# Kernel optimization log

Hardware: AMD Instinct MI355X
Metric: run time of the kernel (lower is better)

Reference implementation:

```python
import jax, jax.numpy as jnp
import numpy as np

N = 8192
NUM_CLASSES = 5
DIM = 3
EPS = 15.0
MIN_POINTS = 5
N_BATCH = 2


def setup_inputs() -> dict:
    key = jax.random.key(0)
    k1, k2, k3, k4 = jax.random.split(key, 4)
    # coords in a 96^3 box so eps=15 neighborhoods contain > minPoints same-group points
    coords = jax.random.uniform(k1, (N, DIM)) * 96.0
    batch = jax.random.randint(k2, (N, 1), 0, N_BATCH).astype(jnp.float32)
    feat = jax.random.normal(k3, (N, 1))
    seg = jax.random.normal(k4, (N, NUM_CLASSES))
    x = jnp.concatenate([coords, batch, feat, seg], axis=1).astype(jnp.float32)
    return {"x": x}


def _dbscan_labels(x):
    """Per-point DBSCAN cluster labels, run independently per (batch, class) group.
    noise = -1; cluster ids start at 0 within each group, ordered by the smallest
    point index of each cluster's core component (matches the serial scan order
    of the original implementation). Border points get the smallest adjacent
    cluster id (= first cluster to reach them in the serial algorithm)."""
    data = x[:, :-NUM_CLASSES]                 # (N, dim+2)
    seg = x[:, -NUM_CLASSES:]                  # (N, C)
    cls = jnp.argmax(seg, axis=1).astype(jnp.int32)
    b = data[:, DIM].astype(jnp.int32)
    pts = data[:, :DIM]                        # (N, 3)
    group = b * NUM_CLASSES + cls              # (N,) group id per point

    # pairwise squared distances via gram trick; d < eps  <=>  d2 < eps^2
    p2 = jnp.sum(pts * pts, axis=1)
    d2 = p2[:, None] + p2[None, :] - 2.0 * (pts @ pts.T)
    same = group[:, None] == group[None, :]
    adj = same & (d2 < EPS * EPS)              # includes self (d2 ~ 0)
    core = jnp.sum(adj, axis=1) >= MIN_POINTS  # region_query counts self too
    adjcc = adj & core[:, None] & core[None, :]

    idx = jnp.arange(N, dtype=jnp.int32)
    SENT = jnp.int32(N)
    lab0 = jnp.where(core, idx, SENT)

    # connected components of core-core graph via min-label propagation + pointer jumping
    def cond(st):
        return st[1]

    def body(st):
        lab, _ = st
        m = jnp.min(jnp.where(adjcc, lab[None, :], SENT), axis=1)
        nl = jnp.minimum(lab, m)
        safe = jnp.where(core, nl, 0)          # nl < N for core points
        nl2 = jnp.where(core, jnp.minimum(nl, nl[safe]), SENT)
        return (nl2, jnp.any(nl2 != lab))

    rep, _ = jax.lax.while_loop(cond, body, (lab0, jnp.array(True)))

    # per-group sequential cluster ids, ordered by component representative index
    is_rep = core & (rep == idx)
    cid_of_rep = jnp.zeros((N,), jnp.int32)
    for g in range(N_BATCH * NUM_CLASSES):     # fixed small count of groups
        mg = is_rep & (group == g)
        cum = jnp.cumsum(mg.astype(jnp.int32))
        cid_of_rep = jnp.where(mg, cum - 1, cid_of_rep)
    core_cid = cid_of_rep[jnp.where(core, rep, 0)]

    # border points: min cluster id among adjacent core points (same group via adj)
    nb_core = adj & core[None, :]
    BIG = jnp.int32(2 ** 30)
    bcid = jnp.min(jnp.where(nb_core, core_cid[None, :], BIG), axis=1)
    has_core_nb = jnp.any(nb_core, axis=1)
    labels = jnp.where(core, core_cid, jnp.where(has_core_nb, bcid, -1))
    return labels


def reference(x):
    labels = _dbscan_labels(x)
    data = x[:, :-NUM_CLASSES]
    # fixed-shape equivalent of the cluster gather: clustered points keep their
    # data columns (the differentiable part of the original output), noise zeroed
    clustered = jnp.where(labels[:, None] >= 0, data, 0.0)
    return labels, clustered
```

## Files before the change

### kernel.cpp

```cpp
#include <hip/hip_runtime.h>
#include <cstdint>
#include <cstddef>

#define NPTS 8192
#define NWORDS 128
#define NUM_CLASSES 5
#define XCOLS 10
#define MIN_PTS 5
#define NGROUPS 10
#define BIGC 0x3fffffff

#define NLCAP 1536
#define EACAP 8192
#define ELCAP 8192
#define EBCAP 2048
#define CPAD 64
#define NSLICE 24
#define PTHREADS 512
#define PWAVES 8
#define GTHREADS 1024
#define ROUNDS 16

__global__ void k_init(const float* __restrict__ x, int* __restrict__ grp,
                       unsigned int* __restrict__ gcnt) {
    int i = blockIdx.x * blockDim.x + threadIdx.x;
    if (i < NGROUPS * CPAD) gcnt[i] = 0u;
    if (i >= NPTS) return;
    const float2* r2 = (const float2*)(x + (size_t)i * XCOLS);
    float2 c23 = r2[1];
    float2 c45 = r2[2];
    float2 c67 = r2[3];
    float2 c89 = r2[4];
    float best = c45.y; int bc = 0;
    if (c67.x > best) { best = c67.x; bc = 1; }
    if (c67.y > best) { best = c67.y; bc = 2; }
    if (c89.x > best) { best = c89.x; bc = 3; }
    if (c89.y > best) { best = c89.y; bc = 4; }
    grp[i] = (int)c23.y * NUM_CLASSES + bc;
}

__global__ void __launch_bounds__(PTHREADS) k_pairs(
        const float* __restrict__ x, const int* __restrict__ grp,
        unsigned int* __restrict__ eAll_g, unsigned int* __restrict__ gcnt,
        int* __restrict__ deg_g, int* __restrict__ nlist_g, int* __restrict__ nn_g) {
    __shared__ float4 pts[NLCAP];
    __shared__ unsigned long long masks[NWORDS];
    __shared__ int pref[NWORDS];
    __shared__ int srowdeg[64];
    __shared__ int nnS;

    const int g = blockIdx.x / NSLICE;
    const int s = blockIdx.x % NSLICE;
    const int tid = threadIdx.x, lane = tid & 63, wv = tid >> 6;

    for (int k = tid; k < NLCAP; k += PTHREADS)
        pts[k] = make_float4(0.f, 0.f, 0.f, 1.0e38f);
    if (tid < 64) srowdeg[tid] = 0;
    for (int w = wv; w < NWORDS; w += PWAVES) {
        unsigned long long bm = __ballot(grp[w * 64 + lane] == g);
        if (lane == 0) masks[w] = bm;
    }
    __syncthreads();
    if (wv == 0) {
        int v0 = __popcll(masks[lane]);
        int incl = v0;
        #pragma unroll
        for (int st = 1; st < 64; st <<= 1) {
            int o = __shfl_up(incl, st);
            if (lane >= st) incl += o;
        }
        pref[lane] = incl - v0;
        int tot0 = __shfl(incl, 63);
        int v1 = __popcll(masks[64 + lane]);
        int incl1 = v1;
        #pragma unroll
        for (int st = 1; st < 64; st <<= 1) {
            int o = __shfl_up(incl1, st);
            if (lane >= st) incl1 += o;
        }
        pref[64 + lane] = tot0 + incl1 - v1;
        if (lane == 63) nnS = tot0 + incl1;
    }
    __syncthreads();
    for (int w = wv; w < NWORDS; w += PWAVES) {
        unsigned long long bm = masks[w];
        if ((bm >> lane) & 1ull) {
            int p = pref[w] + __popcll(bm & ((1ull << lane) - 1ull));
            if (p < NLCAP) {
                int i = w * 64 + lane;
                const float2* r2 = (const float2*)(x + (size_t)i * XCOLS);
                float2 c01 = r2[0]; float2 c23 = r2[1];
                float px = c01.x, py = c01.y, pz = c23.x;
                pts[p] = make_float4(px, py, pz,
                                     0.5f * (px*px + py*py + pz*pz) - 56.25f);
                if (s == 0) nlist_g[g * NLCAP + p] = i;
            }
        }
    }
    if (s == 0 && tid == 0) nn_g[g] = (nnS > NLCAP) ? NLCAP : nnS;
    __syncthreads();
    const int NN = (nnS > NLCAP) ? NLCAP : nnS;

    const int rrow = s + NSLICE * lane;
    const float4 qu = pts[rrow];
    int rdeg = 0;
    const int NC = (NN + 31) >> 5;
    unsigned int* eg = eAll_g + (size_t)g * EACAP;
    for (int c = wv; c < NC; c += PWAVES) {
        int base = c << 5;
        unsigned int bits = 0u;
        #pragma unroll
        for (int t = 0; t < 32; t++) {
            float4 qv = pts[base + t];
            float dt = qu.x*qv.x + qu.y*qv.y + qu.z*qv.z;
            bits |= (dt > qu.w + qv.w) ? (1u << t) : 0u;
        }
        rdeg += __popc(bits);
        int d = rrow - base;
        if (d >= 31) bits = 0u;
        else if (d >= 0) bits &= ~((2u << d) - 1u);
        int cnt = __popc(bits);
        int incl = cnt;
        #pragma unroll
        for (int st = 1; st < 64; st <<= 1) {
            int o = __shfl_up(incl, st);
            if (lane >= st) incl += o;
        }
        int tot = __shfl(incl, 63);
        if (tot > 0) {
            unsigned int rbase = 0;
            if (lane == 63) rbase = atomicAdd(&gcnt[g * CPAD], (unsigned int)tot);
            rbase = __shfl(rbase, 63);
            unsigned int p = rbase + (unsigned int)(incl - cnt);
            unsigned int b = bits;
            unsigned int uhi = (unsigned int)rrow << 11;
            while (b) {
                int t = __ffs(b) - 1; b &= b - 1;
                if (p < EACAP) eg[p] = uhi | (unsigned int)(base + t);
                p++;
            }
        }
    }
    if (rdeg > 0) atomicAdd(&srowdeg[lane], rdeg);
    __syncthreads();
    if (tid < 64)
        deg_g[g * NLCAP + s + NSLICE * tid] = srowdeg[tid];
}

__global__ void __launch_bounds__(GTHREADS) k_graph(
        const unsigned int* __restrict__ eAll_g, const unsigned int* __restrict__ gcnt,
        const int* __restrict__ deg_g, const int* __restrict__ nlist_g,
        const int* __restrict__ nn_g, const float* __restrict__ x,
        float* __restrict__ out) {
    __shared__ unsigned int eL[ELCAP];
    __shared__ unsigned int eB[EBCAP];
    __shared__ int spar[NLCAP];
    __shared__ int scid[NLCAP];
    __shared__ int sbmin[NLCAP];
    __shared__ int nlist[NLCAP];
    __shared__ unsigned long long corebm[NLCAP/64];
    __shared__ unsigned long long repbm[NLCAP/64];
    __shared__ int pref24[NLCAP/64];
    __shared__ int nL, nB;
    __shared__ int sflagA[ROUNDS];

    const int g = blockIdx.x;
    const int tid = threadIdx.x, lane = tid & 63, wv = tid >> 6;
    const int NN = nn_g[g];
    const unsigned int Eu = gcnt[g * CPAD];
    const int NA = (Eu > (unsigned)EACAP) ? EACAP : (int)Eu;
    const unsigned int* eg = eAll_g + (size_t)g * EACAP;

    if (tid == 0) { nL = 0; nB = 0; }
    if (tid < ROUNDS) sflagA[tid] = 0;
    for (int k = tid; k < NLCAP; k += GTHREADS) {
        spar[k] = k;
        sbmin[k] = BIGC;
        nlist[k] = nlist_g[g * NLCAP + k];
    }
    for (int w = wv; w < NLCAP / 64; w += 16) {
        int l = w * 64 + lane;
        bool isc = (l < NN) && (deg_g[g * NLCAP + l] >= MIN_PTS);
        unsigned long long bm = __ballot(isc);
        if (lane == 0) corebm[w] = bm;
    }
    __syncthreads();
    auto corebit = [&](int l) -> bool { return (corebm[l >> 6] >> (l & 63)) & 1ull; };

    for (int e0 = 0; e0 < NA; e0 += GTHREADS) {
        int e = e0 + tid;
        unsigned int pk = (e < NA) ? eg[e] : 0u;
        bool val = (e < NA);
        int u = (int)(pk >> 11), v = (int)(pk & 2047u);
        bool cu = val && corebit(u), cv = val && corebit(v);
        bool isL = cu && cv, isB = val && (cu != cv);
        unsigned long long mL = __ballot(isL);
        if (mL) {
            int b0 = 0;
            if (lane == 0) b0 = atomicAdd(&nL, __popcll(mL));
            b0 = __shfl(b0, 0);
            if (isL) {
                int idx = b0 + __popcll(mL & ((1ull << lane) - 1ull));
                if (idx < ELCAP) eL[idx] = pk;
            }
        }
        unsigned long long mB = __ballot(isB);
        if (mB) {
            int b0 = 0;
            if (lane == 0) b0 = atomicAdd(&nB, __popcll(mB));
            b0 = __shfl(b0, 0);
            if (isB) {
                int idx = b0 + __popcll(mB & ((1ull << lane) - 1ull));
                if (idx < EBCAP) eB[idx] = pk;
            }
        }
    }
    __syncthreads();
    const int NL = (nL > ELCAP) ? ELCAP : nL;
    const int NB = (nB > EBCAP) ? EBCAP : nB;

    for (int r = 0; r < ROUNDS; r++) {
        for (int k = tid; k < NL; k += GTHREADS) {
            unsigned int pk = eL[k];
            int u = (int)(pk >> 11), v = (int)(pk & 2047u);
            int ru = spar[u];
            while (true) { int p = spar[ru]; if (p == ru) break; ru = p; }
            int rv = spar[v];
            while (true) { int p = spar[rv]; if (p == rv) break; rv = p; }
            if (ru < rv)      { if (atomicMin(&spar[rv], ru) > ru) sflagA[r] = 1; }
            else if (rv < ru) { if (atomicMin(&spar[ru], rv) > rv) sflagA[r] = 1; }
        }
        __syncthreads();
        for (int k = tid; k < NN; k += GTHREADS) {
            int p = spar[k];
            while (true) { int q = spar[p]; if (q == p) break; p = q; }
            spar[k] = p;
        }
        __syncthreads();
        if (!sflagA[r]) break;
    }

    for (int w = wv; w < NLCAP / 64; w += 16) {
        int l = w * 64 + lane;
        bool isr = (l < NN) && corebit(l) && (spar[l] == l);
        unsigned long long bm = __ballot(isr);
        if (lane == 0) repbm[w] = bm;
    }
    __syncthreads();
    if (wv == 0 && lane < NLCAP / 64) {
        int c = __popcll(repbm[lane]);
        int incl = c;
        #pragma unroll
        for (int st = 1; st < 32; st <<= 1) {
            int o = __shfl_up(incl, st);
            if (lane >= st) incl += o;
        }
        pref24[lane] = incl - c;
    }
    __syncthreads();
    for (int w = wv; w < NLCAP / 64; w += 16) {
        int l = w * 64 + lane;
        unsigned long long bm = repbm[w];
        if ((bm >> lane) & 1ull)
            scid[l] = pref24[w] + __popcll(bm & ((1ull << lane) - 1ull));
    }
    __syncthreads();
    int cc[2];
    #pragma unroll
    for (int t = 0; t < 2; t++) {
        int k = tid + t * GTHREADS;
        cc[t] = (k < NN && corebit(k)) ? scid[spar[k]] : BIGC;
    }
    __syncthreads();
    #pragma unroll
    for (int t = 0; t < 2; t++) {
        int k = tid + t * GTHREADS;
        if (k < NLCAP) spar[k] = (k < NN) ? cc[t] : BIGC;
    }
    __syncthreads();
    for (int k = tid; k < NB; k += GTHREADS) {
        unsigned int pk = eB[k];
        int u = (int)(pk >> 11), v = (int)(pk & 2047u);
        int cu = spar[u], cv = spar[v];
        if (cu == BIGC) atomicMin(&sbmin[u], cv);
        else            atomicMin(&sbmin[v], cu);
    }
    __syncthreads();
    for (int k = tid; k < NN; k += GTHREADS) {
        int i = nlist[k];
        int c = spar[k];
        int lbl = (c != BIGC) ? c : ((sbmin[k] < BIGC) ? sbmin[k] : -1);
        out[i] = (float)lbl;
        const float* r = x + (size_t)i * XCOLS;
        float* o = out + NPTS + (size_t)i * 5;
        bool keep = lbl >= 0;
        #pragma unroll
        for (int c5 = 0; c5 < 5; c5++) o[c5] = keep ? r[c5] : 0.0f;
    }
}

extern "C" void kernel_launch(void* const* d_in, const int* in_sizes, int n_in,
                              void* d_out, int out_size, void* d_ws, size_t ws_size,
                              hipStream_t stream) {
    const float* x = (const float*)d_in[0];
    float* out = (float*)d_out;
    char* ws = (char*)d_ws;

    int* grp            = (int*)(ws);
    unsigned int* gcnt  = (unsigned int*)(ws + 32768);
    int* nn_g           = (int*)(ws + 35328);
    int* nlist_g        = (int*)(ws + 35392);
    int* deg_g          = (int*)(ws + 96832);
    unsigned int* eAll_g= (unsigned int*)(ws + 158272);

    k_init<<<NPTS / 256, 256, 0, stream>>>(x, grp, gcnt);
    k_pairs<<<NGROUPS * NSLICE, PTHREADS, 0, stream>>>(x, grp, eAll_g, gcnt,
                                                       deg_g, nlist_g, nn_g);
    k_graph<<<NGROUPS, GTHREADS, 0, stream>>>(eAll_g, gcnt, deg_g, nlist_g,
                                              nn_g, x, out);
}
```

Baseline: 92.70 us.

## Fuse init, pair and graph kernels into one per-group block kernel

Merges the three launches into a single kernel with one 1024-thread block per group. The group mask, pair edge list, degrees and neighbor list now stay in shared memory instead of going through global workspace. This removes two launch gaps and the global round trips, but pair testing that used to run across 240 blocks now runs on only 10. Shared memory use per block also grows a lot.

```diff
diff --git a/kernel.cpp b/kernel.cpp
--- a/kernel.cpp
+++ b/kernel.cpp
@@ -4,7 +4,6 @@
 
 #define NPTS 8192
 #define NWORDS 128
-#define NUM_CLASSES 5
 #define XCOLS 10
 #define MIN_PTS 5
 #define NGROUPS 10
@@ -14,50 +13,52 @@
 #define EACAP 8192
 #define ELCAP 8192
 #define EBCAP 2048
-#define CPAD 64
-#define NSLICE 24
-#define PTHREADS 512
-#define PWAVES 8
-#define GTHREADS 1024
+#define NT 1024
+#define NWV 16
 #define ROUNDS 16
 
-__global__ void k_init(const float* __restrict__ x, int* __restrict__ grp,
-                       unsigned int* __restrict__ gcnt) {
-    int i = blockIdx.x * blockDim.x + threadIdx.x;
-    if (i < NGROUPS * CPAD) gcnt[i] = 0u;
-    if (i >= NPTS) return;
-    const float2* r2 = (const float2*)(x + (size_t)i * XCOLS);
-    float2 c23 = r2[1];
-    float2 c45 = r2[2];
-    float2 c67 = r2[3];
-    float2 c89 = r2[4];
-    float best = c45.y; int bc = 0;
-    if (c67.x > best) { best = c67.x; bc = 1; }
-    if (c67.y > best) { best = c67.y; bc = 2; }
-    if (c89.x > best) { best = c89.x; bc = 3; }
-    if (c89.y > best) { best = c89.y; bc = 4; }
-    grp[i] = (int)c23.y * NUM_CLASSES + bc;
-}
-
-__global__ void __launch_bounds__(PTHREADS) k_pairs(
-        const float* __restrict__ x, const int* __restrict__ grp,
-        unsigned int* __restrict__ eAll_g, unsigned int* __restrict__ gcnt,
-        int* __restrict__ deg_g, int* __restrict__ nlist_g, int* __restrict__ nn_g) {
+__global__ void __launch_bounds__(NT) k_all(const float* __restrict__ x,
+                                            float* __restrict__ out) {
     __shared__ float4 pts[NLCAP];
     __shared__ unsigned long long masks[NWORDS];
     __shared__ int pref[NWORDS];
-    __shared__ int srowdeg[64];
-    __shared__ int nnS;
-
-    const int g = blockIdx.x / NSLICE;
-    const int s = blockIdx.x % NSLICE;
+    __shared__ int nlist[NLCAP];
+    __shared__ int sdeg[NLCAP];
+    __shared__ int spar[NLCAP];
+    __shared__ int scid[NLCAP];
+    __shared__ int sbmin[NLCAP];
+    __shared__ unsigned int eA[EACAP];
+    __shared__ unsigned int eL[ELCAP];
+    __shared__ unsigned int eB[EBCAP];
+    __shared__ unsigned int corebm32[NLCAP / 32];
+    __shared__ unsigned long long repbm[NLCAP / 64];
+    __shared__ int pref24[NLCAP / 64];
+    __shared__ int nnS, nA, nL, nB;
+    __shared__ int sflagA[ROUNDS];
+
+    const int g = blockIdx.x;
     const int tid = threadIdx.x, lane = tid & 63, wv = tid >> 6;
 
-    for (int k = tid; k < NLCAP; k += PTHREADS)
+    for (int k = tid; k < NLCAP; k += NT) {
         pts[k] = make_float4(0.f, 0.f, 0.f, 1.0e38f);
-    if (tid < 64) srowdeg[tid] = 0;
-    for (int w = wv; w < NWORDS; w += PWAVES) {
-        unsigned long long bm = __ballot(grp[w * 64 + lane] == g);
+        sdeg[k] = 0; spar[k] = k; sbmin[k] = BIGC;
+    }
+    if (tid == 0) { nA = 0; nL = 0; nB = 0; }
+    if (tid < ROUNDS) sflagA[tid] = 0;
+
+    for (int w = wv; w < NWORDS; w += NWV) {
+        int i = w * 64 + lane;
+        const float2* r2 = (const float2*)(x + (size_t)i * XCOLS);
+        float2 c23 = r2[1];
+        float2 c45 = r2[2];
+        float2 c67 = r2[3];
+        float2 c89 = r2[4];
+        float best = c45.y; int bc = 0;
+        if (c67.x > best) { best = c67.x; bc = 1; }
+        if (c67.y > best) { best = c67.y; bc = 2; }
+        if (c89.x > best) { best = c89.x; bc = 3; }
+        if (c89.y > best) { best = c89.y; bc = 4; }
+        unsigned long long bm = __ballot((int)c23.y * 5 + bc == g);
         if (lane == 0) masks[w] = bm;
     }
     __syncthreads();
@@ -82,7 +83,7 @@
         if (lane == 63) nnS = tot0 + incl1;
     }
     __syncthreads();
-    for (int w = wv; w < NWORDS; w += PWAVES) {
+    for (int w = wv; w < NWORDS; w += NWV) {
         unsigned long long bm = masks[w];
         if ((bm >> lane) & 1ull) {
             int p = pref[w] + __popcll(bm & ((1ull << lane) - 1ull));
@@ -93,103 +94,72 @@
                 float px = c01.x, py = c01.y, pz = c23.x;
                 pts[p] = make_float4(px, py, pz,
                                      0.5f * (px*px + py*py + pz*pz) - 56.25f);
-                if (s == 0) nlist_g[g * NLCAP + p] = i;
-            }
-        }
-    }
-    if (s == 0 && tid == 0) nn_g[g] = (nnS > NLCAP) ? NLCAP : nnS;
-    __syncthreads();
-    const int NN = (nnS > NLCAP) ? NLCAP : nnS;
-
-    const int rrow = s + NSLICE * lane;
-    const float4 qu = pts[rrow];
-    int rdeg = 0;
+                nlist[p] = i;
+            }
+        }
+    }
+    __syncthreads();
+    const int NN = (nnS < NLCAP) ? nnS : NLCAP;
     const int NC = (NN + 31) >> 5;
-    unsigned int* eg = eAll_g + (size_t)g * EACAP;
-    for (int c = wv; c < NC; c += PWAVES) {
-        int base = c << 5;
-        unsigned int bits = 0u;
-        #pragma unroll
-        for (int t = 0; t < 32; t++) {
-            float4 qv = pts[base + t];
-            float dt = qu.x*qv.x + qu.y*qv.y + qu.z*qv.z;
-            bits |= (dt > qu.w + qv.w) ? (1u << t) : 0u;
-        }
-        rdeg += __popc(bits);
-        int d = rrow - base;
-        if (d >= 31) bits = 0u;
-        else if (d >= 0) bits &= ~((2u << d) - 1u);
-        int cnt = __popc(bits);
-        int incl = cnt;
-        #pragma unroll
-        for (int st = 1; st < 64; st <<= 1) {
-            int o = __shfl_up(incl, st);
-            if (lane >= st) incl += o;
-        }
-        int tot = __shfl(incl, 63);
-        if (tot > 0) {
-            unsigned int rbase = 0;
-            if (lane == 63) rbase = atomicAdd(&gcnt[g * CPAD], (unsigned int)tot);
-            rbase = __shfl(rbase, 63);
-            unsigned int p = rbase + (unsigned int)(incl - cnt);
-            unsigned int b = bits;
-            unsigned int uhi = (unsigned int)rrow << 11;
-            while (b) {
-                int t = __ffs(b) - 1; b &= b - 1;
-                if (p < EACAP) eg[p] = uhi | (unsigned int)(base + t);
-                p++;
-            }
-        }
-    }
-    if (rdeg > 0) atomicAdd(&srowdeg[lane], rdeg);
-    __syncthreads();
-    if (tid < 64)
-        deg_g[g * NLCAP + s + NSLICE * tid] = srowdeg[tid];
-}
-
-__global__ void __launch_bounds__(GTHREADS) k_graph(
-        const unsigned int* __restrict__ eAll_g, const unsigned int* __restrict__ gcnt,
-        const int* __restrict__ deg_g, const int* __restrict__ nlist_g,
-        const int* __restrict__ nn_g, const float* __restrict__ x,
-        float* __restrict__ out) {
-    __shared__ unsigned int eL[ELCAP];
-    __shared__ unsigned int eB[EBCAP];
-    __shared__ int spar[NLCAP];
-    __shared__ int scid[NLCAP];
-    __shared__ int sbmin[NLCAP];
-    __shared__ int nlist[NLCAP];
-    __shared__ unsigned long long corebm[NLCAP/64];
-    __shared__ unsigned long long repbm[NLCAP/64];
-    __shared__ int pref24[NLCAP/64];
-    __shared__ int nL, nB;
-    __shared__ int sflagA[ROUNDS];
-
-    const int g = blockIdx.x;
-    const int tid = threadIdx.x, lane = tid & 63, wv = tid >> 6;
-    const int NN = nn_g[g];
-    const unsigned int Eu = gcnt[g * CPAD];
-    const int NA = (Eu > (unsigned)EACAP) ? EACAP : (int)Eu;
-    const unsigned int* eg = eAll_g + (size_t)g * EACAP;
-
-    if (tid == 0) { nL = 0; nB = 0; }
-    if (tid < ROUNDS) sflagA[tid] = 0;
-    for (int k = tid; k < NLCAP; k += GTHREADS) {
-        spar[k] = k;
-        sbmin[k] = BIGC;
-        nlist[k] = nlist_g[g * NLCAP + k];
-    }
-    for (int w = wv; w < NLCAP / 64; w += 16) {
-        int l = w * 64 + lane;
-        bool isc = (l < NN) && (deg_g[g * NLCAP + l] >= MIN_PTS);
-        unsigned long long bm = __ballot(isc);
-        if (lane == 0) corebm[w] = bm;
-    }
-    __syncthreads();
-    auto corebit = [&](int l) -> bool { return (corebm[l >> 6] >> (l & 63)) & 1ull; };
-
-    for (int e0 = 0; e0 < NA; e0 += GTHREADS) {
+
+    for (int rb = 0; rb < NLCAP; rb += NT) {
+        if (rb + (wv << 6) >= NN) break;
+        int r = rb + tid;
+        float4 qu = pts[r];
+        int rdeg = 0;
+        for (int c = 0; c < NC; c++) {
+            int base = c << 5;
+            unsigned int bits = 0u;
+            #pragma unroll
+            for (int t = 0; t < 32; t++) {
+                float4 qv = pts[base + t];
+                float dt = qu.x*qv.x + qu.y*qv.y + qu.z*qv.z;
+                bits |= (dt > qu.w + qv.w) ? (1u << t) : 0u;
+            }
+            rdeg += __popc(bits);
+            int d = r - base;
+            if (d >= 31) bits = 0u;
+            else if (d >= 0) bits &= ~((2u << d) - 1u);
+            int cnt = __popc(bits);
+            int incl = cnt;
+            #pragma unroll
+            for (int st = 1; st < 64; st <<= 1) {
+                int o = __shfl_up(incl, st);
+                if (lane >= st) incl += o;
+            }
+            int tot = __shfl(incl, 63);
+            if (tot > 0) {
+                int rbse = 0;
+                if (lane == 63) rbse = atomicAdd(&nA, tot);
+                rbse = __shfl(rbse, 63);
+                unsigned int p = (unsigned int)(rbse + incl - cnt);
+                unsigned int b = bits;
+                unsigned int uhi = (unsigned int)r << 11;
+                while (b) {
+                    int t = __ffs(b) - 1; b &= b - 1;
+                    if (p < EACAP) eA[p] = uhi | (unsigned int)(base + t);
+                    p++;
+                }
+            }
+        }
+        sdeg[r] = rdeg;
+    }
+    __syncthreads();
+    const int NA = (nA > EACAP) ? EACAP : nA;
+
+    for (int wd = tid; wd < NLCAP / 32; wd += NT) {
+        unsigned int m = 0u;
+        #pragma unroll
+        for (int j = 0; j < 32; j++)
+            m |= (sdeg[wd * 32 + j] >= MIN_PTS) ? (1u << j) : 0u;
+        corebm32[wd] = m;
+    }
+    __syncthreads();
+    auto corebit = [&](int l) -> bool { return (corebm32[l >> 5] >> (l & 31)) & 1u; };
+
+    for (int e0 = 0; e0 < NA; e0 += NT) {
         int e = e0 + tid;
-        unsigned int pk = (e < NA) ? eg[e] : 0u;
+        unsigned int pk = (e < NA) ? eA[e] : 0u;
         bool val = (e < NA);
         int u = (int)(pk >> 11), v = (int)(pk & 2047u);
         bool cu = val && corebit(u), cv = val && corebit(v);
@@ -220,7 +190,7 @@
     const int NB = (nB > EBCAP) ? EBCAP : nB;
 
     for (int r = 0; r < ROUNDS; r++) {
-        for (int k = tid; k < NL; k += GTHREADS) {
+        for (int k = tid; k < NL; k += NT) {
             unsigned int pk = eL[k];
             int u = (int)(pk >> 11), v = (int)(pk & 2047u);
             int ru = spar[u];
@@ -231,7 +201,7 @@
             else if (rv < ru) { if (atomicMin(&spar[ru], rv) > rv) sflagA[r] = 1; }
         }
         __syncthreads();
-        for (int k = tid; k < NN; k += GTHREADS) {
+        for (int k = tid; k < NN; k += NT) {
             int p = spar[k];
             while (true) { int q = spar[p]; if (q == p) break; p = q; }
             spar[k] = p;
@@ -240,7 +210,7 @@
         if (!sflagA[r]) break;
     }
 
-    for (int w = wv; w < NLCAP / 64; w += 16) {
+    for (int w = wv; w < NLCAP / 64; w += NWV) {
         int l = w * 64 + lane;
         bool isr = (l < NN) && corebit(l) && (spar[l] == l);
         unsigned long long bm = __ballot(isr);
@@ -258,7 +228,7 @@
         pref24[lane] = incl - c;
     }
     __syncthreads();
-    for (int w = wv; w < NLCAP / 64; w += 16) {
+    for (int w = wv; w < NLCAP / 64; w += NWV) {
         int l = w * 64 + lane;
         unsigned long long bm = repbm[w];
         if ((bm >> lane) & 1ull)
@@ -268,17 +238,17 @@
     int cc[2];
     #pragma unroll
     for (int t = 0; t < 2; t++) {
-        int k = tid + t * GTHREADS;
+        int k = tid + t * NT;
         cc[t] = (k < NN && corebit(k)) ? scid[spar[k]] : BIGC;
     }
     __syncthreads();
     #pragma unroll
     for (int t = 0; t < 2; t++) {
-        int k = tid + t * GTHREADS;
+        int k = tid + t * NT;
         if (k < NLCAP) spar[k] = (k < NN) ? cc[t] : BIGC;
     }
     __syncthreads();
-    for (int k = tid; k < NB; k += GTHREADS) {
+    for (int k = tid; k < NB; k += NT) {
         unsigned int pk = eB[k];
         int u = (int)(pk >> 11), v = (int)(pk & 2047u);
         int cu = spar[u], cv = spar[v];
@@ -286,7 +256,7 @@
         else            atomicMin(&sbmin[v], cu);
     }
     __syncthreads();
-    for (int k = tid; k < NN; k += GTHREADS) {
+    for (int k = tid; k < NN; k += NT) {
         int i = nlist[k];
         int c = spar[k];
         int lbl = (c != BIGC) ? c : ((sbmin[k] < BIGC) ? sbmin[k] : -1);
@@ -304,18 +274,6 @@
                               hipStream_t stream) {
     const float* x = (const float*)d_in[0];
     float* out = (float*)d_out;
-    char* ws = (char*)d_ws;
-
-    int* grp            = (int*)(ws);
-    unsigned int* gcnt  = (unsigned int*)(ws + 32768);
-    int* nn_g           = (int*)(ws + 35328);
-    int* nlist_g        = (int*)(ws + 35392);
-    int* deg_g          = (int*)(ws + 96832);
-    unsigned int* eAll_g= (unsigned int*)(ws + 158272);
-
-    k_init<<<NPTS / 256, 256, 0, stream>>>(x, grp, gcnt);
-    k_pairs<<<NGROUPS * NSLICE, PTHREADS, 0, stream>>>(x, grp, eAll_g, gcnt,
-                                                       deg_g, nlist_g, nn_g);
-    k_graph<<<NGROUPS, GTHREADS, 0, stream>>>(eAll_g, gcnt, deg_g, nlist_g,
-                                              nn_g, x, out);
+    (void)d_ws; (void)ws_size;
+    k_all<<<NGROUPS, NT, 0, stream>>>(x, out);
 }
```

New measurement: 128.5 us. 38.7% more time.
